# Kernel optimization log

Hardware: AMD Instinct MI355X
Metric: run time of the kernel (lower is better)

## Reference

```python
import jax, jax.numpy as jnp
import numpy as np

B, N, S, D1, D2 = 16, 4096, 1024, 128, 256
MLP = [256, 128]
BN_EPS = 1e-5


def setup_inputs() -> dict:
    key = jax.random.key(0)
    ks = jax.random.split(key, 12)
    inp = {
        "xyz1": jax.random.normal(ks[0], (B, 3, N), dtype=jnp.float32),
        "xyz2": jax.random.normal(ks[1], (B, 3, S), dtype=jnp.float32),
        "points1": jax.random.normal(ks[2], (B, D1, N), dtype=jnp.float32),
        "points2": jax.random.normal(ks[3], (B, D2, S), dtype=jnp.float32),
    }
    in_ch = D1 + D2  # 384
    chans = [in_ch] + MLP
    ki = 4
    for li in range(len(MLP)):
        cin, cout = chans[li], chans[li + 1]
        inp[f"w{li+1}"] = jax.random.normal(ks[ki], (cout, cin), dtype=jnp.float32) * (1.0 / np.sqrt(cin)); ki += 1
        inp[f"b{li+1}"] = jnp.zeros((cout,), dtype=jnp.float32)
        inp[f"g{li+1}"] = jnp.ones((cout,), dtype=jnp.float32)
        inp[f"beta{li+1}"] = jnp.zeros((cout,), dtype=jnp.float32)
    return inp


def _batchnorm1d(x, gamma, beta):
    # x: [B, C, N]; training-mode batch stats over (B, N)
    mean = jnp.mean(x, axis=(0, 2), keepdims=True)
    var = jnp.var(x, axis=(0, 2), keepdims=True)
    xhat = (x - mean) * jax.lax.rsqrt(var + BN_EPS)
    return xhat * gamma[None, :, None] + beta[None, :, None]


def reference(xyz1, xyz2, points1, points2, w1, b1, g1, beta1, w2, b2, g2, beta2):
    x1 = jnp.transpose(xyz1, (0, 2, 1))   # [B, N, 3]
    x2 = jnp.transpose(xyz2, (0, 2, 1))   # [B, S, 3]
    p2 = jnp.transpose(points2, (0, 2, 1))  # [B, S, D2]

    # squared pairwise distances [B, N, S]
    dists = jnp.sum((x1[:, :, None, :] - x2[:, None, :, :]) ** 2, axis=-1)
    # 3 smallest distances (original sorts then slices top-3)
    neg_d3, idx = jax.lax.top_k(-dists, 3)  # [B, N, 3]
    d3 = -neg_d3
    dist_recip = 1.0 / (d3 + 1e-8)
    weight = dist_recip / jnp.sum(dist_recip, axis=2, keepdims=True)  # [B, N, 3]

    # gather neighbor features: [B, N, 3, D2]
    feats = p2[jnp.arange(p2.shape[0])[:, None, None], idx]
    interp = jnp.sum(feats * weight[..., None], axis=2)  # [B, N, D2]

    p1 = jnp.transpose(points1, (0, 2, 1))  # [B, N, D1]
    new_points = jnp.concatenate([p1, interp], axis=-1)  # [B, N, D1+D2]
    x = jnp.transpose(new_points, (0, 2, 1))  # [B, C, N]

    for w, b, g, bt in ((w1, b1, g1, beta1), (w2, b2, g2, beta2)):
        x = jnp.einsum("oc,bcn->bon", w, x) + b[None, :, None]
        x = _batchnorm1d(x, g, bt)
        x = jax.nn.relu(x)
    return x
```

## Files before the change

### kernel.cpp

```cpp
#include <hip/hip_runtime.h>

typedef unsigned short u16;
typedef unsigned int   u32;
typedef unsigned long long u64;
typedef __attribute__((ext_vector_type(8))) short bf16x8;
typedef __attribute__((ext_vector_type(8))) unsigned short u16x8;
typedef __attribute__((ext_vector_type(4))) float f32x4;

#define NB   16
#define NPTS 4096
#define SPTS 1024
#define BNT  65536

#define G2L(src, dst) __builtin_amdgcn_global_load_lds( \
    (const __attribute__((address_space(1))) void*)(src), \
    (__attribute__((address_space(3))) void*)(dst), 16, 0, 0)

__device__ __forceinline__ float bf2f(u16 u){ return __uint_as_float(((u32)u)<<16); }
__device__ __forceinline__ u16 f2bf(float f){
  u32 u = __float_as_uint(f);
  return (u16)((u + 0x7FFFu + ((u>>16)&1u))>>16);
}

__global__ __launch_bounds__(256) void convw_k(const float* __restrict__ w1, const float* __restrict__ w2,
                                               u16* __restrict__ w1b, u16* __restrict__ w2b){
  int i = blockIdx.x*256 + threadIdx.x;
  if (i < 98304) w1b[i] = f2bf(w1[i]);
  else { int j = i - 98304; w2b[j] = f2bf(w2[j]); }
}

__global__ __launch_bounds__(256) void transpose_k(const float* __restrict__ in, u16* __restrict__ out,
                                                   int C, int S, int ostride){
  __shared__ float tl[64][65];
  int t = threadIdx.x;
  int b = blockIdx.y;
  int s0 = blockIdx.x * 64;
  for (int ct = 0; ct < C; ct += 64){
    __syncthreads();
    for (int i = t; i < 4096; i += 256){
      int sl = i & 63, cl = i >> 6;
      tl[sl][cl] = in[((size_t)b*C + ct + cl)*S + s0 + sl];
    }
    __syncthreads();
    for (int i = t; i < 4096; i += 256){
      int cl = i & 63, sl = i >> 6;
      out[((size_t)b*S + s0 + sl)*ostride + ct + cl] = f2bf(tl[sl][cl]);
    }
  }
}

__global__ __launch_bounds__(512) void knn_k(const float* __restrict__ xyz1, const float* __restrict__ xyz2,
                                             const u16* __restrict__ p2t, u16* __restrict__ X){
  __shared__ float4 sxyz[SPTS];
  __shared__ double pp[16][3][32];
  __shared__ float  swts[3][32];
  __shared__ int    sidx[3][32];
  int t  = threadIdx.x;
  int b  = blockIdx.x >> 7;
  int n0 = (blockIdx.x & 127) << 5;
  const float* x2b = xyz2 + (size_t)b*3*SPTS;
  for (int s = t; s < SPTS; s += 512)
    sxyz[s] = make_float4(x2b[s], x2b[SPTS+s], x2b[2*SPTS+s], 0.f);
  int q = t & 31, g = t >> 5;
  const float* x1b = xyz1 + (size_t)b*3*NPTS;
  int n = n0 + q;
  float qx = x1b[n], qy = x1b[NPTS+n], qz = x1b[2*NPTS+n];
  __syncthreads();

  double k0 = 1e300, k1 = 1e300, k2 = 1e300;
  int sBeg = g << 6;
  #pragma unroll 4
  for (int sj = 0; sj < 64; ++sj){
    int s = sBeg + sj;
    float4 p = sxyz[s];
    float dist;
    {
      #pragma clang fp contract(off)
      float dx = qx - p.x, dy = qy - p.y, dz = qz - p.z;
      dist = ((dx*dx) + (dy*dy)) + (dz*dz);
    }
    double pk = __longlong_as_double(__double_as_longlong((double)dist) | (long long)s);
    double n2 = fmin(fmax(pk, k1), k2);
    double n1 = fmin(fmax(pk, k0), k1);
    double n0d = fmin(pk, k0);
    k0 = n0d; k1 = n1; k2 = n2;
  }
  pp[g][0][q] = k0; pp[g][1][q] = k1; pp[g][2][q] = k2;
  __syncthreads();

  if (t < 32){
    double m0 = 1e300, m1 = 1e300, m2 = 1e300;
    #pragma unroll
    for (int gg = 0; gg < 16; ++gg){
      #pragma unroll
      for (int p = 0; p < 3; ++p){
        double pk = pp[gg][p][t];
        double n2 = fmin(fmax(pk, m1), m2);
        double n1 = fmin(fmax(pk, m0), m1);
        double n0d = fmin(pk, m0);
        m0 = n0d; m1 = n1; m2 = n2;
      }
    }
    int j0 = (int)(__double_as_longlong(m0) & 1023);
    int j1 = (int)(__double_as_longlong(m1) & 1023);
    int j2 = (int)(__double_as_longlong(m2) & 1023);
    float e0 = (float)m0, e1 = (float)m1, e2 = (float)m2;
    float r0 = 1.f/(e0 + 1e-8f), r1 = 1.f/(e1 + 1e-8f), r2 = 1.f/(e2 + 1e-8f);
    float rs = (r0 + r1) + r2;
    swts[0][t] = r0/rs; swts[1][t] = r1/rs; swts[2][t] = r2/rs;
    sidx[0][t] = j0;    sidx[1][t] = j1;    sidx[2][t] = j2;
  }
  __syncthreads();

  int w = t >> 6, lane = t & 63;
  for (int qq = w*4; qq < w*4 + 4; ++qq){
    float wa = swts[0][qq], wb = swts[1][qq], wc = swts[2][qq];
    int   j0 = sidx[0][qq], j1 = sidx[1][qq], j2 = sidx[2][qq];
    const ushort4 u0 = *(const ushort4*)(p2t + (((size_t)b*SPTS + j0)<<8) + (lane<<2));
    const ushort4 u1 = *(const ushort4*)(p2t + (((size_t)b*SPTS + j1)<<8) + (lane<<2));
    const ushort4 u2 = *(const ushort4*)(p2t + (((size_t)b*SPTS + j2)<<8) + (lane<<2));
    ushort4 ov;
    ov.x = f2bf(wa*bf2f(u0.x) + wb*bf2f(u1.x) + wc*bf2f(u2.x));
    ov.y = f2bf(wa*bf2f(u0.y) + wb*bf2f(u1.y) + wc*bf2f(u2.y));
    ov.z = f2bf(wa*bf2f(u0.z) + wb*bf2f(u1.z) + wc*bf2f(u2.z));
    ov.w = f2bf(wa*bf2f(u0.w) + wb*bf2f(u1.w) + wc*bf2f(u2.w));
    *(ushort4*)(X + ((size_t)b*NPTS + n0 + qq)*384 + 128 + (lane<<2)) = ov;
  }
}

__global__ __launch_bounds__(256) void gemm1_k(const u16* __restrict__ A, const u16* __restrict__ Bw,
                                               u16* __restrict__ Cc,
                                               float* __restrict__ psum, float* __restrict__ psq){
  const int K = 384, Nn = 256;
  __shared__ u16 lA[2][64*32];
  __shared__ u16 lB[2][256*32];
  float* sums = (float*)lA;
  float* sqs  = sums + 256;
  int t = threadIdx.x, lane = t & 63, wid = t >> 6;
  int rowBase = blockIdx.x << 6;
  int wm = wid >> 1, wn = wid & 1;

  const char* pA; int dAo;
  {
    int L = t*16;
    int row = L >> 6, kb = L & 63;
    int kbs = kb ^ ((row & 3) << 4);
    pA = (const char*)A + (size_t)(rowBase + row)*768 + kbs;
    dAo = wid*1024;
  }
  const char* pB[4]; int dBo[4];
  #pragma unroll
  for (int j = 0; j < 4; ++j){
    int L = j*4096 + t*16;
    int row = L >> 6, kb = L & 63;
    int kbs = kb ^ ((row & 3) << 4);
    pB[j] = (const char*)Bw + (size_t)row*768 + kbs;
    dBo[j] = j*4096 + wid*1024;
  }

  f32x4 z = {0.f,0.f,0.f,0.f};
  f32x4 acc[2][8];
  #pragma unroll
  for (int m = 0; m < 2; ++m)
    #pragma unroll
    for (int n = 0; n < 8; ++n) acc[m][n] = z;

  G2L(pA, (char*)lA[0] + dAo);
  #pragma unroll
  for (int j = 0; j < 4; ++j) G2L(pB[j], (char*)lB[0] + dBo[j]);
  __syncthreads();

  #pragma unroll
  for (int kt = 0; kt < 12; ++kt){
    const int cur = kt & 1;
    if (kt < 11){
      size_t ko = (size_t)(kt + 1) * 64;
      G2L(pA + ko, (char*)lA[cur^1] + dAo);
      #pragma unroll
      for (int j = 0; j < 4; ++j) G2L(pB[j] + ko, (char*)lB[cur^1] + dBo[j]);
    }
    bf16x8 af[2];
    #pragma unroll
    for (int m = 0; m < 2; ++m){
      int row = wm*32 + m*16 + (lane & 15);
      int kb = ((lane >> 4) << 4) ^ ((row & 3) << 4);
      af[m] = *(const bf16x8*)((const char*)lA[cur] + row*64 + kb);
    }
    #pragma unroll
    for (int n = 0; n < 8; ++n){
      int row = wn*128 + n*16 + (lane & 15);
      int kb = ((lane >> 4) << 4) ^ ((row & 3) << 4);
      bf16x8 bv = *(const bf16x8*)((const char*)lB[cur] + row*64 + kb);
      acc[0][n] = __builtin_amdgcn_mfma_f32_16x16x32_bf16(af[0], bv, acc[0][n], 0, 0, 0);
      acc[1][n] = __builtin_amdgcn_mfma_f32_16x16x32_bf16(af[1], bv, acc[1][n], 0, 0, 0);
    }
    __syncthreads();
  }

  sums[t] = 0.f; sqs[t] = 0.f;
  __syncthreads();
  int colb = wn*128 + (lane & 15);
  int rowb = rowBase + wm*32 + ((lane >> 4) << 2);
  #pragma unroll
  for (int n = 0; n < 8; ++n){
    float s = 0.f, qq2 = 0.f;
    #pragma unroll
    for (int m = 0; m < 2; ++m){
      #pragma unroll
      for (int r = 0; r < 4; ++r){
        float v = acc[m][n][r];
        Cc[(size_t)(rowb + m*16 + r)*Nn + colb + n*16] = f2bf(v);
        s += v; qq2 += v*v;
      }
    }
    atomicAdd(&sums[colb + n*16], s);
    atomicAdd(&sqs [colb + n*16], qq2);
  }
  __syncthreads();
  psum[(size_t)t*1024 + blockIdx.x] = sums[t];
  psq [(size_t)t*1024 + blockIdx.x] = sqs[t];
}

__global__ __launch_bounds__(256) void gemm2_k(const u16* __restrict__ A, const u16* __restrict__ Bw,
                                               u16* __restrict__ Cc,
                                               const float* __restrict__ sc, const float* __restrict__ sh,
                                               float* __restrict__ psum, float* __restrict__ psq){
  const int K = 256, Nn = 128;
  __shared__ u16 lA[64*64];
  __shared__ u16 lB[128*64];
  __shared__ float sums[128], sqs[128];
  int t = threadIdx.x, lane = t & 63, wid = t >> 6;
  int rowBase = blockIdx.x << 6;
  int wm = wid >> 1, wn = wid & 1;

  const char* pB[4]; int dBo[4];
  #pragma unroll
  for (int j = 0; j < 4; ++j){
    int L = j*4096 + t*16;
    int row = L >> 7, kb = L & 127;
    int kbs = kb ^ ((row & 7) << 4);
    pB[j] = (const char*)Bw + ((size_t)row*K)*2 + kbs;
    dBo[j] = j*4096 + wid*1024;
  }
  int arow = t & 63, achunk = t >> 6;
  const u16* pArow = A + (size_t)(rowBase + arow)*K + achunk*16;
  int asw = (arow & 7) << 4;
  char* wA0 = (char*)lA + arow*128 + ((achunk*32)      ^ asw);
  char* wA1 = (char*)lA + arow*128 + ((achunk*32 + 16) ^ asw);

  f32x4 z = {0.f,0.f,0.f,0.f};
  f32x4 acc[2][4];
  #pragma unroll
  for (int m = 0; m < 2; ++m)
    #pragma unroll
    for (int n = 0; n < 4; ++n) acc[m][n] = z;

  for (int kk = 0; kk < K; kk += 64){
    size_t ko = (size_t)kk * 2;
    #pragma unroll
    for (int j = 0; j < 4; ++j) G2L(pB[j] + ko, (char*)lB + dBo[j]);
    u16x8 y0 = *(const u16x8*)(pArow + kk);
    u16x8 y1 = *(const u16x8*)(pArow + kk + 8);
    int k0 = kk + achunk*16;
    bf16x8 o0, o1;
    #pragma unroll
    for (int j = 0; j < 8; ++j){
      float v = bf2f((u16)y0[j]) * sc[k0 + j] + sh[k0 + j];
      o0[j] = (short)f2bf(fmaxf(v, 0.f));
    }
    #pragma unroll
    for (int j = 0; j < 8; ++j){
      float v = bf2f((u16)y1[j]) * sc[k0 + 8 + j] + sh[k0 + 8 + j];
      o1[j] = (short)f2bf(fmaxf(v, 0.f));
    }
    *(bf16x8*)wA0 = o0;
    *(bf16x8*)wA1 = o1;
    __syncthreads();
    bf16x8 af[2][2], bfv[4][2];
    #pragma unroll
    for (int m = 0; m < 2; ++m){
      int row = wm*32 + m*16 + (lane & 15);
      int sw = (row & 7) << 4;
      #pragma unroll
      for (int ks = 0; ks < 2; ++ks){
        int kb = (ks*64 + ((lane >> 4) << 4)) ^ sw;
        af[m][ks] = *(const bf16x8*)((const char*)lA + row*128 + kb);
      }
    }
    #pragma unroll
    for (int n = 0; n < 4; ++n){
      int row = wn*64 + n*16 + (lane & 15);
      int sw = (row & 7) << 4;
      #pragma unroll
      for (int ks = 0; ks < 2; ++ks){
        int kb = (ks*64 + ((lane >> 4) << 4)) ^ sw;
        bfv[n][ks] = *(const bf16x8*)((const char*)lB + row*128 + kb);
      }
    }
    #pragma unroll
    for (int ks = 0; ks < 2; ++ks)
      #pragma unroll
      for (int m = 0; m < 2; ++m)
        #pragma unroll
        for (int n = 0; n < 4; ++n)
          acc[m][n] = __builtin_amdgcn_mfma_f32_16x16x32_bf16(af[m][ks], bfv[n][ks], acc[m][n], 0, 0, 0);
    __syncthreads();
  }

  if (t < 128){ sums[t] = 0.f; sqs[t] = 0.f; }
  __syncthreads();
  int colb = wn*64 + (lane & 15);
  int rowb = rowBase + wm*32 + ((lane >> 4) << 2);
  #pragma unroll
  for (int n = 0; n < 4; ++n){
    float s = 0.f, qq2 = 0.f;
    #pragma unroll
    for (int m = 0; m < 2; ++m){
      #pragma unroll
      for (int r = 0; r < 4; ++r){
        float v = acc[m][n][r];
        Cc[(size_t)(rowb + m*16 + r)*Nn + colb + n*16] = f2bf(v);
        s += v; qq2 += v*v;
      }
    }
    atomicAdd(&sums[colb + n*16], s);
    atomicAdd(&sqs [colb + n*16], qq2);
  }
  __syncthreads();
  if (t < 128){
    psum[(size_t)t*1024 + blockIdx.x] = sums[t];
    psq [(size_t)t*1024 + blockIdx.x] = sqs[t];
  }
}

__global__ __launch_bounds__(256) void finalize2_k(const float* __restrict__ psum, const float* __restrict__ psq,
                                                   const float* __restrict__ g, const float* __restrict__ bet,
                                                   float* __restrict__ sc, float* __restrict__ sh){
  __shared__ float rs[256], rq[256];
  int c = blockIdx.x, t = threadIdx.x;
  float s = 0.f, q = 0.f;
  for (int rt = t; rt < 1024; rt += 256){
    s += psum[(size_t)c*1024 + rt];
    q += psq [(size_t)c*1024 + rt];
  }
  rs[t] = s; rq[t] = q;
  __syncthreads();
  for (int off = 128; off; off >>= 1){
    if (t < off){ rs[t] += rs[t+off]; rq[t] += rq[t+off]; }
    __syncthreads();
  }
  if (t == 0){
    const float inv = 1.f/65536.f;
    float mean = rs[0]*inv;
    float var  = rq[0]*inv - mean*mean;
    float rstd = rsqrtf(var + 1e-5f);
    float scl  = g[c]*rstd;
    sc[c] = scl;
    sh[c] = bet[c] - mean*scl;
  }
}

__global__ __launch_bounds__(256) void finalout_k(const u16* __restrict__ y2, const float* __restrict__ sc,
                                                  const float* __restrict__ sh, float* __restrict__ out){
  __shared__ float tl[128][65];
  int t  = threadIdx.x;
  int b  = blockIdx.x >> 6;
  int n0 = (blockIdx.x & 63) << 6;
  for (int i = t; i < 8192; i += 256){
    int r = i >> 7, c = i & 127;
    float v = bf2f(y2[((size_t)b*NPTS + n0 + r)*128 + c]);
    v = fmaxf(v*sc[c] + sh[c], 0.f);
    tl[c][r] = v;
  }
  __syncthreads();
  for (int i = t; i < 8192; i += 256){
    int o = i >> 6, j = i & 63;
    out[(size_t)b*128*NPTS + (size_t)o*NPTS + n0 + j] = tl[o][j];
  }
}

extern "C" void kernel_launch(void* const* d_in, const int* in_sizes, int n_in,
                              void* d_out, int out_size, void* d_ws, size_t ws_size,
                              hipStream_t stream) {
  const float* xyz1    = (const float*)d_in[0];
  const float* xyz2    = (const float*)d_in[1];
  const float* points1 = (const float*)d_in[2];
  const float* points2 = (const float*)d_in[3];
  const float* w1      = (const float*)d_in[4];
  const float* g1      = (const float*)d_in[6];
  const float* beta1   = (const float*)d_in[7];
  const float* w2      = (const float*)d_in[8];
  const float* g2      = (const float*)d_in[10];
  const float* beta2   = (const float*)d_in[11];

  char* ws = (char*)d_ws;
  u16*  X    = (u16*)ws;
  u16*  Y2   = (u16*)ws;
  u16*  Y1   = (u16*)(ws + 50331648);
  u16*  p2t  = (u16*)(ws + 83886080);
  u16*  w1b  = (u16*)(ws + 92274688);
  u16*  w2b  = (u16*)(ws + 92471296);
  float* psum1 = (float*)(ws + 83886080);
  float* psq1  = (float*)(ws + 84934656);
  float* psum2 = (float*)(ws + 85983232);
  float* psq2  = (float*)(ws + 86507520);
  float* sc1   = (float*)(ws + 87031808);
  float* sh1   = (float*)(ws + 87032832);
  float* sc2   = (float*)(ws + 87033856);
  float* sh2   = (float*)(ws + 87034368);

  convw_k<<<512, 256, 0, stream>>>(w1, w2, w1b, w2b);
  transpose_k<<<dim3(64, 16), 256, 0, stream>>>(points1, X,   128, NPTS, 384);
  transpose_k<<<dim3(16, 16), 256, 0, stream>>>(points2, p2t, 256, SPTS, 256);
  knn_k<<<2048, 512, 0, stream>>>(xyz1, xyz2, p2t, X);
  gemm1_k<<<1024, 256, 0, stream>>>(X, w1b, Y1, psum1, psq1);
  finalize2_k<<<256, 256, 0, stream>>>(psum1, psq1, g1, beta1, sc1, sh1);
  gemm2_k<<<1024, 256, 0, stream>>>(Y1, w2b, Y2, sc1, sh1, psum2, psq2);
  finalize2_k<<<128, 256, 0, stream>>>(psum2, psq2, g2, beta2, sc2, sh2);
  finalout_k<<<1024, 256, 0, stream>>>(Y2, sc2, sh2, (float*)d_out);
}
```

Measured before the change: 159.9 us.

## Apply W1 interp half to points2 before KNN interpolation, shrinking gemm1 K

Because interpolation is linear, the W1 columns acting on interpolated features are applied to the 1024 source points (a new small GEMM producing Z) instead of the 4096 query points. The KNN kernel then interpolates the projected 256-wide Z rows directly into a Y1 partial buffer. gemm1 drops to K=128 over points1 and adds that partial in its epilogue. This cuts GEMM FLOPs and the 384-wide concatenated buffer, at the cost of an extra kernel, an extra bf16 rounding of the partial, and removal of gemm1's double buffering.

Measured after the change: 164.7 us. 1.03x slower.

```diff
diff --git a/kernel.cpp b/kernel.cpp
--- a/kernel.cpp
+++ b/kernel.cpp
@@ -2,7 +2,6 @@
 
 typedef unsigned short u16;
 typedef unsigned int   u32;
-typedef unsigned long long u64;
 typedef __attribute__((ext_vector_type(8))) short bf16x8;
 typedef __attribute__((ext_vector_type(8))) unsigned short u16x8;
 typedef __attribute__((ext_vector_type(4))) float f32x4;
@@ -23,10 +22,19 @@
 }
 
 __global__ __launch_bounds__(256) void convw_k(const float* __restrict__ w1, const float* __restrict__ w2,
-                                               u16* __restrict__ w1b, u16* __restrict__ w2b){
+                                               u16* __restrict__ w1aa, u16* __restrict__ w1bb,
+                                               u16* __restrict__ w2b){
   int i = blockIdx.x*256 + threadIdx.x;
-  if (i < 98304) w1b[i] = f2bf(w1[i]);
-  else { int j = i - 98304; w2b[j] = f2bf(w2[j]); }
+  if (i < 32768){
+    int c = i >> 7, k = i & 127;
+    w1aa[i] = f2bf(w1[c*384 + k]);
+  } else if (i < 98304){
+    int j = i - 32768; int c = j >> 8, k = j & 255;
+    w1bb[j] = f2bf(w1[c*384 + 128 + k]);
+  } else {
+    int j = i - 98304;
+    w2b[j] = f2bf(w2[j]);
+  }
 }
 
 __global__ __launch_bounds__(256) void transpose_k(const float* __restrict__ in, u16* __restrict__ out,
@@ -49,8 +57,78 @@
   }
 }
 
+__global__ __launch_bounds__(256) void zgemm_k(const u16* __restrict__ A, const u16* __restrict__ Bw,
+                                               u16* __restrict__ Zc){
+  const int Nn = 256;
+  __shared__ u16 lA[64*32];
+  __shared__ u16 lB[256*32];
+  int t = threadIdx.x, lane = t & 63, wid = t >> 6;
+  int rowBase = blockIdx.x << 6;
+  int wm = wid >> 1, wn = wid & 1;
+
+  const char* pA; int dAo;
+  {
+    int L = t*16;
+    int row = L >> 6, slot = (L & 63) >> 4;
+    int kbs = (slot ^ ((row >> 1) & 3)) << 4;
+    pA = (const char*)A + (size_t)(rowBase + row)*512 + kbs;
+    dAo = wid*1024;
+  }
+  const char* pB[4]; int dBo[4];
+  #pragma unroll
+  for (int j = 0; j < 4; ++j){
+    int L = j*4096 + t*16;
+    int row = L >> 6, slot = (L & 63) >> 4;
+    int kbs = (slot ^ ((row >> 1) & 3)) << 4;
+    pB[j] = (const char*)Bw + (size_t)row*512 + kbs;
+    dBo[j] = j*4096 + wid*1024;
+  }
+
+  f32x4 z = {0.f,0.f,0.f,0.f};
+  f32x4 acc[2][8];
+  #pragma unroll
+  for (int m = 0; m < 2; ++m)
+    #pragma unroll
+    for (int n = 0; n < 8; ++n) acc[m][n] = z;
+
+  #pragma unroll
+  for (int kt = 0; kt < 8; ++kt){
+    size_t ko = (size_t)kt * 64;
+    G2L(pA + ko, (char*)lA + dAo);
+    #pragma unroll
+    for (int j = 0; j < 4; ++j) G2L(pB[j] + ko, (char*)lB + dBo[j]);
+    __syncthreads();
+    bf16x8 af[2];
+    #pragma unroll
+    for (int m = 0; m < 2; ++m){
+      int row = wm*32 + m*16 + (lane & 15);
+      int kb = ((lane >> 4) ^ ((row >> 1) & 3)) << 4;
+      af[m] = *(const bf16x8*)((const char*)lA + row*64 + kb);
+    }
+    #pragma unroll
+    for (int n = 0; n < 8; ++n){
+      int row = wn*128 + n*16 + (lane & 15);
+      int kb = ((lane >> 4) ^ ((row >> 1) & 3)) << 4;
+      bf16x8 bv = *(const bf16x8*)((const char*)lB + row*64 + kb);
+      acc[0][n] = __builtin_amdgcn_mfma_f32_16x16x32_bf16(af[0], bv, acc[0][n], 0, 0, 0);
+      acc[1][n] = __builtin_amdgcn_mfma_f32_16x16x32_bf16(af[1], bv, acc[1][n], 0, 0, 0);
+    }
+    __syncthreads();
+  }
+
+  int colb = wn*128 + (lane & 15);
+  int rowb = rowBase + wm*32 + ((lane >> 4) << 2);
+  #pragma unroll
+  for (int n = 0; n < 8; ++n)
+    #pragma unroll
+    for (int m = 0; m < 2; ++m)
+      #pragma unroll
+      for (int r = 0; r < 4; ++r)
+        Zc[(size_t)(rowb + m*16 + r)*Nn + colb + n*16] = f2bf(acc[m][n][r]);
+}
+
 __global__ __launch_bounds__(512) void knn_k(const float* __restrict__ xyz1, const float* __restrict__ xyz2,
-                                             const u16* __restrict__ p2t, u16* __restrict__ X){
+                                             const u16* __restrict__ zt, u16* __restrict__ Y1b){
   __shared__ float4 sxyz[SPTS];
   __shared__ double pp[16][3][32];
   __shared__ float  swts[3][32];
@@ -116,26 +194,25 @@
   for (int qq = w*4; qq < w*4 + 4; ++qq){
     float wa = swts[0][qq], wb = swts[1][qq], wc = swts[2][qq];
     int   j0 = sidx[0][qq], j1 = sidx[1][qq], j2 = sidx[2][qq];
-    const ushort4 u0 = *(const ushort4*)(p2t + (((size_t)b*SPTS + j0)<<8) + (lane<<2));
-    const ushort4 u1 = *(const ushort4*)(p2t + (((size_t)b*SPTS + j1)<<8) + (lane<<2));
-    const ushort4 u2 = *(const ushort4*)(p2t + (((size_t)b*SPTS + j2)<<8) + (lane<<2));
+    const ushort4 u0 = *(const ushort4*)(zt + (((size_t)b*SPTS + j0)<<8) + (lane<<2));
+    const ushort4 u1 = *(const ushort4*)(zt + (((size_t)b*SPTS + j1)<<8) + (lane<<2));
+    const ushort4 u2 = *(const ushort4*)(zt + (((size_t)b*SPTS + j2)<<8) + (lane<<2));
     ushort4 ov;
     ov.x = f2bf(wa*bf2f(u0.x) + wb*bf2f(u1.x) + wc*bf2f(u2.x));
     ov.y = f2bf(wa*bf2f(u0.y) + wb*bf2f(u1.y) + wc*bf2f(u2.y));
     ov.z = f2bf(wa*bf2f(u0.z) + wb*bf2f(u1.z) + wc*bf2f(u2.z));
     ov.w = f2bf(wa*bf2f(u0.w) + wb*bf2f(u1.w) + wc*bf2f(u2.w));
-    *(ushort4*)(X + ((size_t)b*NPTS + n0 + qq)*384 + 128 + (lane<<2)) = ov;
+    *(ushort4*)(Y1b + (((size_t)b*NPTS + n0 + qq)<<8) + (lane<<2)) = ov;
   }
 }
 
 __global__ __launch_bounds__(256) void gemm1_k(const u16* __restrict__ A, const u16* __restrict__ Bw,
-                                               u16* __restrict__ Cc,
+                                               const u16* __restrict__ Y1b, u16* __restrict__ Cc,
                                                float* __restrict__ psum, float* __restrict__ psq){
-  const int K = 384, Nn = 256;
-  __shared__ u16 lA[2][64*32];
-  __shared__ u16 lB[2][256*32];
-  float* sums = (float*)lA;
-  float* sqs  = sums + 256;
+  const int Nn = 256;
+  __shared__ u16 lA[64*32];
+  __shared__ u16 lB[256*32];
+  __shared__ float sums[256], sqs[256];
   int t = threadIdx.x, lane = t & 63, wid = t >> 6;
   int rowBase = blockIdx.x << 6;
   int wm = wid >> 1, wn = wid & 1;
@@ -143,18 +220,18 @@
   const char* pA; int dAo;
   {
     int L = t*16;
-    int row = L >> 6, kb = L & 63;
-    int kbs = kb ^ ((row & 3) << 4);
-    pA = (const char*)A + (size_t)(rowBase + row)*768 + kbs;
+    int row = L >> 6, slot = (L & 63) >> 4;
+    int kbs = (slot ^ ((row >> 1) & 3)) << 4;
+    pA = (const char*)A + (size_t)(rowBase + row)*256 + kbs;
     dAo = wid*1024;
   }
   const char* pB[4]; int dBo[4];
   #pragma unroll
   for (int j = 0; j < 4; ++j){
     int L = j*4096 + t*16;
-    int row = L >> 6, kb = L & 63;
-    int kbs = kb ^ ((row & 3) << 4);
-    pB[j] = (const char*)Bw + (size_t)row*768 + kbs;
+    int row = L >> 6, slot = (L & 63) >> 4;
+    int kbs = (slot ^ ((row >> 1) & 3)) << 4;
+    pB[j] = (const char*)Bw + (size_t)row*256 + kbs;
     dBo[j] = j*4096 + wid*1024;
   }
 
@@ -165,32 +242,25 @@
     #pragma unroll
     for (int n = 0; n < 8; ++n) acc[m][n] = z;
 
-  G2L(pA, (char*)lA[0] + dAo);
-  #pragma unroll
-  for (int j = 0; j < 4; ++j) G2L(pB[j], (char*)lB[0] + dBo[j]);
-  __syncthreads();
-
-  #pragma unroll
-  for (int kt = 0; kt < 12; ++kt){
-    const int cur = kt & 1;
-    if (kt < 11){
-      size_t ko = (size_t)(kt + 1) * 64;
-      G2L(pA + ko, (char*)lA[cur^1] + dAo);
-      #pragma unroll
-      for (int j = 0; j < 4; ++j) G2L(pB[j] + ko, (char*)lB[cur^1] + dBo[j]);
-    }
+  #pragma unroll
+  for (int kt = 0; kt < 4; ++kt){
+    size_t ko = (size_t)kt * 64;
+    G2L(pA + ko, (char*)lA + dAo);
+    #pragma unroll
+    for (int j = 0; j < 4; ++j) G2L(pB[j] + ko, (char*)lB + dBo[j]);
+    __syncthreads();
     bf16x8 af[2];
     #pragma unroll
     for (int m = 0; m < 2; ++m){
       int row = wm*32 + m*16 + (lane & 15);
-      int kb = ((lane >> 4) << 4) ^ ((row & 3) << 4);
-      af[m] = *(const bf16x8*)((const char*)lA[cur] + row*64 + kb);
+      int kb = ((lane >> 4) ^ ((row >> 1) & 3)) << 4;
+      af[m] = *(const bf16x8*)((const char*)lA + row*64 + kb);
     }
     #pragma unroll
     for (int n = 0; n < 8; ++n){
       int row = wn*128 + n*16 + (lane & 15);
-      int kb = ((lane >> 4) << 4) ^ ((row & 3) << 4);
-      bf16x8 bv = *(const bf16x8*)((const char*)lB[cur] + row*64 + kb);
+      int kb = ((lane >> 4) ^ ((row >> 1) & 3)) << 4;
+      bf16x8 bv = *(const bf16x8*)((const char*)lB + row*64 + kb);
       acc[0][n] = __builtin_amdgcn_mfma_f32_16x16x32_bf16(af[0], bv, acc[0][n], 0, 0, 0);
       acc[1][n] = __builtin_amdgcn_mfma_f32_16x16x32_bf16(af[1], bv, acc[1][n], 0, 0, 0);
     }
@@ -208,8 +278,9 @@
     for (int m = 0; m < 2; ++m){
       #pragma unroll
       for (int r = 0; r < 4; ++r){
-        float v = acc[m][n][r];
-        Cc[(size_t)(rowb + m*16 + r)*Nn + colb + n*16] = f2bf(v);
+        size_t off = (size_t)(rowb + m*16 + r)*Nn + colb + n*16;
+        float v = acc[m][n][r] + bf2f(Y1b[off]);
+        Cc[off] = f2bf(v);
         s += v; qq2 += v*v;
       }
     }
@@ -394,12 +465,12 @@
   const float* beta2   = (const float*)d_in[11];
 
   char* ws = (char*)d_ws;
-  u16*  X    = (u16*)ws;
+  u16*  P1   = (u16*)ws;
   u16*  Y2   = (u16*)ws;
+  u16*  Y1b  = (u16*)(ws + 16777216);
+  u16*  Z    = (u16*)(ws + 50331648);
   u16*  Y1   = (u16*)(ws + 50331648);
   u16*  p2t  = (u16*)(ws + 83886080);
-  u16*  w1b  = (u16*)(ws + 92274688);
-  u16*  w2b  = (u16*)(ws + 92471296);
   float* psum1 = (float*)(ws + 83886080);
   float* psq1  = (float*)(ws + 84934656);
   float* psum2 = (float*)(ws + 85983232);
@@ -408,12 +479,16 @@
   float* sh1   = (float*)(ws + 87032832);
   float* sc2   = (float*)(ws + 87033856);
   float* sh2   = (float*)(ws + 87034368);
-
-  convw_k<<<512, 256, 0, stream>>>(w1, w2, w1b, w2b);
-  transpose_k<<<dim3(64, 16), 256, 0, stream>>>(points1, X,   128, NPTS, 384);
+  u16*  w1aa = (u16*)(ws + 92274688);
+  u16*  w1bb = (u16*)(ws + 92340224);
+  u16*  w2b  = (u16*)(ws + 92471296);
+
+  convw_k<<<512, 256, 0, stream>>>(w1, w2, w1aa, w1bb, w2b);
+  transpose_k<<<dim3(64, 16), 256, 0, stream>>>(points1, P1,  128, NPTS, 128);
   transpose_k<<<dim3(16, 16), 256, 0, stream>>>(points2, p2t, 256, SPTS, 256);
-  knn_k<<<2048, 512, 0, stream>>>(xyz1, xyz2, p2t, X);
-  gemm1_k<<<1024, 256, 0, stream>>>(X, w1b, Y1, psum1, psq1);
+  zgemm_k<<<256, 256, 0, stream>>>(p2t, w1bb, Z);
+  knn_k<<<2048, 512, 0, stream>>>(xyz1, xyz2, Z, Y1b);
+  gemm1_k<<<1024, 256, 0, stream>>>(P1, w1aa, Y1b, Y1, psum1, psq1);
   finalize2_k<<<256, 256, 0, stream>>>(psum1, psq1, g1, beta1, sc1, sh1);
   gemm2_k<<<1024, 256, 0, stream>>>(Y1, w2b, Y2, sc1, sh1, psum2, psq2);
   finalize2_k<<<128, 256, 0, stream>>>(psum2, psq2, g2, beta2, sc2, sh2);
```
